# Performance work log

Hardware: AMD Instinct MI355X
Metric: run time of the kernel (lower is better)

The kernel has to match this reference:

```python
import jax, jax.numpy as jnp
import numpy as np

N_NODES = 30000
NEG_SLOPE = 0.2  # PyG GATConv default leaky_relu slope


def gat_conv(x, src, dst, W, a_src, a_dst, b, num_nodes, concat):
    """One PyG-style GATConv layer (add_self_loops already applied to src/dst).
    x: [N, F_in]; W: [F_in, H*C]; a_src, a_dst: [H, C]; b: [H*C] or [C].
    """
    H, C = a_src.shape
    h = (x @ W).reshape(num_nodes, H, C)                     # [N, H, C]
    alpha_src = jnp.einsum('nhc,hc->nh', h, a_src)           # [N, H]
    alpha_dst = jnp.einsum('nhc,hc->nh', h, a_dst)           # [N, H]
    e = jax.nn.leaky_relu(alpha_src[src] + alpha_dst[dst], NEG_SLOPE)  # [E, H]
    # scatter-softmax over incoming edges of each dst node
    e_max = jax.ops.segment_max(e, dst, num_segments=num_nodes)        # [N, H]
    e_exp = jnp.exp(e - e_max[dst])                                    # [E, H]
    denom = jax.ops.segment_sum(e_exp, dst, num_segments=num_nodes)    # [N, H]
    alpha = e_exp / denom[dst]                                         # [E, H]
    msg = h[src] * alpha[:, :, None]                                   # [E, H, C]
    out = jax.ops.segment_sum(msg, dst, num_segments=num_nodes)        # [N, H, C]
    out = out.reshape(num_nodes, H * C) if concat else out.mean(axis=1)
    return out + b


def _glorot(key, shape):
    fan = sum(shape[:2]) if len(shape) > 1 else shape[0] * 2
    return jax.random.normal(key, shape, dtype=jnp.float32) * np.sqrt(2.0 / fan)


def setup_inputs() -> dict:
    key = jax.random.key(0)
    ks = jax.random.split(key, 16)
    n, f_in, heads = N_NODES, 256, 4
    x = jax.random.normal(ks[0], (n, f_in), dtype=jnp.float32)
    edge_index = jax.random.randint(ks[1], (2, 480000), 0, n, dtype=jnp.int64)
    inp = {
        'x': x, 'edge_index': edge_index,
        'W1': _glorot(ks[2], (f_in, heads * 128)),
        'a1s': _glorot(ks[3], (heads, 128)), 'a1d': _glorot(ks[4], (heads, 128)),
        'b1': jnp.zeros((heads * 128,), jnp.float32),
        'W2': _glorot(ks[5], (heads * 128, heads * 128)),
        'a2s': _glorot(ks[6], (heads, 128)), 'a2d': _glorot(ks[7], (heads, 128)),
        'b2': jnp.zeros((heads * 128,), jnp.float32),
        'W3': _glorot(ks[8], (heads * 128, heads * 64)),
        'a3s': _glorot(ks[9], (heads, 64)), 'a3d': _glorot(ks[10], (heads, 64)),
        'b3': jnp.zeros((heads * 64,), jnp.float32),
        # conv4: 256 -> 64, 1 head, mean (concat=False)
        'W4': _glorot(ks[11], (heads * 64, 64)),
        'a4s': _glorot(ks[12], (1, 64)), 'a4d': _glorot(ks[13], (1, 64)),
        'b4': jnp.zeros((64,), jnp.float32),
    }
    return inp


def reference(x, edge_index, W1, a1s, a1d, b1, W2, a2s, a2d, b2,
              W3, a3s, a3d, b3, W4, a4s, a4d, b4):
    n = x.shape[0]
    # PyG GATConv default add_self_loops=True
    loops = jnp.arange(n, dtype=edge_index.dtype)
    src = jnp.concatenate([edge_index[0], loops])
    dst = jnp.concatenate([edge_index[1], loops])
    h = jax.nn.relu(gat_conv(x, src, dst, W1, a1s, a1d, b1, n, True))
    h = jax.nn.relu(gat_conv(h, src, dst, W2, a2s, a2d, b2, n, True))
    h = jax.nn.relu(gat_conv(h, src, dst, W3, a3s, a3d, b3, n, True))
    h = jax.nn.relu(gat_conv(h, src, dst, W4, a4s, a4d, b4, n, False))
    return h
```

## Files before the change

### kernel.cpp

```cpp
#include <hip/hip_runtime.h>
#include <hip/hip_fp16.h>
#include <math.h>


typedef __attribute__((ext_vector_type(8))) _Float16 f16x8;
typedef __attribute__((ext_vector_type(4))) float floatx4;
typedef __attribute__((ext_vector_type(8))) unsigned short usv8;
typedef __attribute__((ext_vector_type(4))) unsigned short usv4;

#define DEG_CAP 256

__device__ __forceinline__ float lrelu(float e) {
    return (e > 0.f) ? e : 0.2f * e;
}
__device__ __forceinline__ void gload16(const void* g, void* l) {
    __builtin_amdgcn_global_load_lds(
        (const __attribute__((address_space(1))) void*)g,
        (__attribute__((address_space(3))) void*)l, 16, 0, 0);
}

static __global__ void zero_int(int* __restrict__ p, int n) {
    int i = blockIdx.x * blockDim.x + threadIdx.x;
    if (i < n) p[i] = 0;
}

static __global__ void hist_kernel(const int* __restrict__ ei, int e0, int n_nodes,
                                   int* __restrict__ counts) {
    int e = blockIdx.x * blockDim.x + threadIdx.x;
    int et = e0 + n_nodes;
    if (e >= et) return;
    int d = (e < e0) ? ei[e0 + e] : (e - e0);
    atomicAdd(&counts[d], 1);
}

static __global__ void scan_kernel(const int* __restrict__ counts,
                                   int* __restrict__ row_ptr,
                                   int* __restrict__ cursor, int n) {
    __shared__ int sdata[1024];
    int tid = threadIdx.x;
    int per = (n + 1023) / 1024;
    int start = tid * per;
    int stop = min(start + per, n);
    if (start > n) start = n;
    int s = 0;
    for (int i = start; i < stop; i++) s += counts[i];
    sdata[tid] = s;
    __syncthreads();
    for (int off = 1; off < 1024; off <<= 1) {
        int t = (tid >= off) ? sdata[tid - off] : 0;
        __syncthreads();
        sdata[tid] += t;
        __syncthreads();
    }
    int run = sdata[tid] - s;
    for (int i = start; i < stop; i++) {
        row_ptr[i] = run;
        cursor[i] = run;
        run += counts[i];
    }
    if (stop == n) row_ptr[n] = run;
}

static __global__ void scatter_kernel(const int* __restrict__ ei, int e0, int n_nodes,
                                      int* __restrict__ cursor,
                                      int* __restrict__ src_sorted) {
    int e = blockIdx.x * blockDim.x + threadIdx.x;
    int et = e0 + n_nodes;
    if (e >= et) return;
    int s, d;
    if (e < e0) { s = ei[e]; d = ei[e0 + e]; } else { s = e - e0; d = s; }
    int pos = atomicAdd(&cursor[d], 1);
    src_sorted[pos] = s;
}

__device__ __forceinline__ void convW_one(const float* W, __half* BT,
                                          int idx, int K, int N) {
    int n = idx / K, k = idx % K;
    float v = (n < N) ? W[(size_t)k * N + n] : 0.f;
    BT[(size_t)n * K + k] = __float2half(v);
}

static __global__ void conv_all(const float* __restrict__ X, __half* __restrict__ A, int nx,
                                const float* __restrict__ W1, __half* __restrict__ BT1,
                                const float* __restrict__ W2, __half* __restrict__ BT2,
                                const float* __restrict__ W3, __half* __restrict__ BT3,
                                const float* __restrict__ W4, __half* __restrict__ BT4,
                                float* __restrict__ zero_as, int nzero) {
    int idx = blockIdx.x * 256 + threadIdx.x;
    if (idx < nx) { A[idx] = __float2half(X[idx]); return; }
    idx -= nx;
    if (idx < 131072) { convW_one(W1, BT1, idx, 256, 512); return; }
    idx -= 131072;
    if (idx < 262144) { convW_one(W2, BT2, idx, 512, 512); return; }
    idx -= 262144;
    if (idx < 131072) { convW_one(W3, BT3, idx, 512, 256); return; }
    idx -= 131072;
    if (idx < 32768)  { convW_one(W4, BT4, idx, 256, 64); return; }
    idx -= 32768;
    if (idx < nzero) zero_as[idx] = 0.f;
}

#define BM 128
#define BN 128
#define BKK 64

__launch_bounds__(256, 4)
static __global__ void gemm_mfma(const __half* __restrict__ A,
                                 const __half* __restrict__ B,
                                 __half* __restrict__ C, int M, int K, int N,
                                 int xcols, int mblocks,
                                 const float* __restrict__ asv,
                                 const float* __restrict__ adv,
                                 float* __restrict__ as_out,
                                 float* __restrict__ ad_out,
                                 int Hh, int Cc) {
    __shared__ __align__(16) __half lds[2 * BM * BKK];
    const int tid  = threadIdx.x;
    const int lane = tid & 63;
    const int wave = tid >> 6;

    const int id = blockIdx.x;
    const int band = id / (8 * xcols);
    const int rem = id - band * 8 * xcols;
    const int band_rows = min(8, mblocks - band * 8);
    const int ry = rem % band_rows;
    const int rx = rem / band_rows;
    const int r0 = (band * 8 + ry) * BM;
    const int c0 = rx * BN;

    const int wm = (wave >> 1) * 64;
    const int wn = (wave & 1) * 64;
    const int q   = lane >> 4;
    const int m16 = lane & 15;

    floatx4 acc[4][4];
#pragma unroll
    for (int i = 0; i < 4; i++)
#pragma unroll
        for (int j = 0; j < 4; j++) acc[i][j] = {0.f, 0.f, 0.f, 0.f};

    char* ldsb = (char*)lds;

#pragma unroll 1
    for (int k0 = 0; k0 < K; k0 += BKK) {
        __syncthreads();
#pragma unroll
        for (int c = 0; c < 4; c++) {
            int slot = c * 256 + tid;
            int row = slot >> 3;
            int gc  = (slot & 7) ^ (row & 7);
            gload16(A + (size_t)(r0 + row) * K + k0 + gc * 8,
                    ldsb + slot * 16);
            gload16(B + (size_t)(c0 + row) * K + k0 + gc * 8,
                    ldsb + 16384 + slot * 16);
        }
        __syncthreads();
#pragma unroll
        for (int ks = 0; ks < 2; ks++) {
            f16x8 af[4], bf[4];
#pragma unroll
            for (int i = 0; i < 4; i++) {
                int row = wm + i * 16 + m16;
                int ch  = (q + ks * 4) ^ (row & 7);
                af[i] = *(const f16x8*)(ldsb + (row * 8 + ch) * 16);
            }
#pragma unroll
            for (int j = 0; j < 4; j++) {
                int row = wn + j * 16 + m16;
                int ch  = (q + ks * 4) ^ (row & 7);
                bf[j] = *(const f16x8*)(ldsb + 16384 + (row * 8 + ch) * 16);
            }
#pragma unroll
            for (int i = 0; i < 4; i++)
#pragma unroll
                for (int j = 0; j < 4; j++)
                    acc[i][j] = __builtin_amdgcn_mfma_f32_16x16x32_f16(
                        af[i], bf[j], acc[i][j], 0, 0, 0);
        }
    }
#pragma unroll
    for (int i = 0; i < 4; i++)
#pragma unroll
        for (int j = 0; j < 4; j++)
#pragma unroll
            for (int r = 0; r < 4; r++) {
                int row = r0 + wm + i * 16 + q * 4 + r;
                int col = c0 + wn + j * 16 + m16;
                if (row < M && col < N)
                    C[(size_t)row * N + col] = __float2half(acc[i][j][r]);
            }
    if (c0 + wn < N) {
        int head = (c0 + wn) / Cc;
#pragma unroll
        for (int i = 0; i < 4; i++)
#pragma unroll
            for (int r = 0; r < 4; r++) {
                float ps = 0.f, pd = 0.f;
#pragma unroll
                for (int j = 0; j < 4; j++) {
                    int c = c0 + wn + j * 16 + m16;
                    float v = acc[i][j][r];
                    ps = fmaf(v, asv[c], ps);
                    pd = fmaf(v, adv[c], pd);
                }
#pragma unroll
                for (int off = 1; off < 16; off <<= 1) {
                    ps += __shfl_xor(ps, off);
                    pd += __shfl_xor(pd, off);
                }
                if (m16 == 0) {
                    int row = r0 + wm + i * 16 + q * 4 + r;
                    if (row < M) {
                        atomicAdd(&as_out[(size_t)row * Hh + head], ps);
                        atomicAdd(&ad_out[(size_t)row * Hh + head], pd);
                    }
                }
            }
    }
}

template <int R>
__device__ __forceinline__ void accum_row(const __half* hptr, size_t off, float w,
                                          float* acc) {
    const __half* p = hptr + off;
    if constexpr (R == 8) {
        float4 raw = *(const float4*)p;
        const __half* hv = (const __half*)&raw;
#pragma unroll
        for (int r = 0; r < 8; r++) acc[r] = fmaf(__half2float(hv[r]), w, acc[r]);
    } else if constexpr (R == 4) {
        float2 raw = *(const float2*)p;
        const __half* hv = (const __half*)&raw;
#pragma unroll
        for (int r = 0; r < 4; r++) acc[r] = fmaf(__half2float(hv[r]), w, acc[r]);
    } else {
        acc[0] = fmaf(__half2float(*p), w, acc[0]);
    }
}

template <int H, int C, bool F16OUT>
__launch_bounds__(256)
static __global__ void agg_kernel(const __half* __restrict__ h,
                                  const float* __restrict__ as_arr,
                                  const float* __restrict__ ad_arr,
                                  const int* __restrict__ row_ptr,
                                  const int* __restrict__ src_sorted,
                                  const float* __restrict__ bias,
                                  float* __restrict__ outf,
                                  __half* __restrict__ outh,
                                  float* __restrict__ znext_as,
                                  float* __restrict__ znext_ad, int n_nodes) {
    constexpr int R = H * C / 64;
    constexpr int G = 64 / H;
    constexpr int K = H * C;
    __shared__ float lds_e[4][DEG_CAP * H];
    int wave = threadIdx.x >> 6;
    int lane = threadIdx.x & 63;
    int n = blockIdx.x * 4 + wave;
    if (n >= n_nodes) return;
    int beg = row_ptr[n], end = row_ptr[n + 1];
    float* we = lds_e[wave];

    float ad_h[H], m_h[H], l_h[H];
#pragma unroll
    for (int hh = 0; hh < H; hh++) {
        ad_h[hh] = ad_arr[(size_t)n * H + hh];
        m_h[hh] = -INFINITY;
        l_h[hh] = 0.f;
    }
    for (int base = beg; base < end; base += 64) {
        int j = base + lane;
        bool ok = j < end;
        float e_h[H];
        if (ok) {
            int s = src_sorted[j];
            if constexpr (H == 4) {
                float4 a = ((const float4*)as_arr)[s];
                e_h[0] = lrelu(a.x + ad_h[0]);
                e_h[1] = lrelu(a.y + ad_h[1]);
                e_h[2] = lrelu(a.z + ad_h[2]);
                e_h[3] = lrelu(a.w + ad_h[3]);
            } else {
                e_h[0] = lrelu(as_arr[s] + ad_h[0]);
            }
            int idx = j - beg;
            if (idx < DEG_CAP) {
                if constexpr (H == 4) {
                    *(float4*)&we[idx * 4] = make_float4(e_h[0], e_h[1], e_h[2], e_h[3]);
                } else {
                    we[idx] = e_h[0];
                }
            }
        } else {
#pragma unroll
            for (int hh = 0; hh < H; hh++) e_h[hh] = -INFINITY;
        }
#pragma unroll
        for (int hh = 0; hh < H; hh++) {
            float cm = e_h[hh];
#pragma unroll
            for (int off = 1; off < 64; off <<= 1) cm = fmaxf(cm, __shfl_xor(cm, off));
            float newm = fmaxf(m_h[hh], cm);
            float p = ok ? __expf(e_h[hh] - newm) : 0.f;
#pragma unroll
            for (int off = 1; off < 64; off <<= 1) p += __shfl_xor(p, off);
            l_h[hh] = l_h[hh] * __expf(m_h[hh] - newm) + p;
            m_h[hh] = newm;
        }
    }
    int myh = lane / G;
    float mm, adm, inv;
    if constexpr (H == 4) {
        mm  = m_h[0];  mm  = (myh == 1) ? m_h[1] : mm;  mm  = (myh == 2) ? m_h[2] : mm;  mm  = (myh == 3) ? m_h[3] : mm;
        float ll = l_h[0]; ll = (myh == 1) ? l_h[1] : ll; ll = (myh == 2) ? l_h[2] : ll; ll = (myh == 3) ? l_h[3] : ll;
        adm = ad_h[0]; adm = (myh == 1) ? ad_h[1] : adm; adm = (myh == 2) ? ad_h[2] : adm; adm = (myh == 3) ? ad_h[3] : adm;
        inv = 1.f / ll;
    } else {
        mm = m_h[0]; adm = ad_h[0]; inv = 1.f / l_h[0];
    }

    float acc[R];
#pragma unroll
    for (int r = 0; r < R; r++) acc[r] = 0.f;

    int j = beg;
    for (; j + 3 < end; j += 4) {
        int i0 = j - beg;
        int s0 = src_sorted[j];
        int s1 = src_sorted[j + 1];
        int s2 = src_sorted[j + 2];
        int s3 = src_sorted[j + 3];
        float e0, e1, e2, e3;
        if (i0 + 3 < DEG_CAP) {
            e0 = we[(i0 + 0) * H + myh];
            e1 = we[(i0 + 1) * H + myh];
            e2 = we[(i0 + 2) * H + myh];
            e3 = we[(i0 + 3) * H + myh];
        } else {
            e0 = lrelu(as_arr[(size_t)s0 * H + myh] + adm);
            e1 = lrelu(as_arr[(size_t)s1 * H + myh] + adm);
            e2 = lrelu(as_arr[(size_t)s2 * H + myh] + adm);
            e3 = lrelu(as_arr[(size_t)s3 * H + myh] + adm);
        }
        float w0 = __expf(e0 - mm) * inv;
        float w1 = __expf(e1 - mm) * inv;
        float w2 = __expf(e2 - mm) * inv;
        float w3 = __expf(e3 - mm) * inv;
        accum_row<R>(h, (size_t)s0 * K + lane * R, w0, acc);
        accum_row<R>(h, (size_t)s1 * K + lane * R, w1, acc);
        accum_row<R>(h, (size_t)s2 * K + lane * R, w2, acc);
        accum_row<R>(h, (size_t)s3 * K + lane * R, w3, acc);
    }
    for (; j < end; j++) {
        int i0 = j - beg;
        int s0 = src_sorted[j];
        float e0 = (i0 < DEG_CAP) ? we[i0 * H + myh]
                                  : lrelu(as_arr[(size_t)s0 * H + myh] + adm);
        float w0 = __expf(e0 - mm) * inv;
        accum_row<R>(h, (size_t)s0 * K + lane * R, w0, acc);
    }

    if (znext_as != nullptr && lane == 0) {
        if constexpr (H == 4) {
            *(float4*)&znext_as[(size_t)n * 4] = make_float4(0.f, 0.f, 0.f, 0.f);
            *(float4*)&znext_ad[(size_t)n * 4] = make_float4(0.f, 0.f, 0.f, 0.f);
        } else {
            znext_as[n] = 0.f;
            znext_ad[n] = 0.f;
        }
    }
    float vout[R];
#pragma unroll
    for (int r = 0; r < R; r++)
        vout[r] = fmaxf(acc[r] + bias[lane * R + r], 0.f);

    if constexpr (F16OUT) {
        unsigned short hv[R];
#pragma unroll
        for (int r = 0; r < R; r++)
            hv[r] = __half_as_ushort(__float2half(vout[r]));
        size_t base = (size_t)n * K + lane * R;
        if constexpr (R == 8) {
            usv8 v = {hv[0], hv[1], hv[2], hv[3], hv[4], hv[5], hv[6], hv[7]};
            *(usv8*)((unsigned short*)outh + base) = v;
        } else if constexpr (R == 4) {
            usv4 v = {hv[0], hv[1], hv[2], hv[3]};
            *(usv4*)((unsigned short*)outh + base) = v;
        } else {
#pragma unroll
            for (int r = 0; r < R; r++) ((unsigned short*)outh)[base + r] = hv[r];
        }
    } else {
#pragma unroll
        for (int r = 0; r < R; r++)
            outf[(size_t)n * K + lane * R + r] = vout[r];
    }
}


static inline size_t align_up(size_t x) { return (x + 255) & ~(size_t)255; }

extern "C" void kernel_launch(void* const* d_in, const int* in_sizes, int n_in,
                              void* d_out, int out_size, void* d_ws, size_t ws_size,
                              hipStream_t stream) {
    const float* x   = (const float*)d_in[0];
    const int*   ei  = (const int*)d_in[1];
    const float* W1  = (const float*)d_in[2];
    const float* a1s = (const float*)d_in[3];
    const float* a1d = (const float*)d_in[4];
    const float* b1  = (const float*)d_in[5];
    const float* W2  = (const float*)d_in[6];
    const float* a2s = (const float*)d_in[7];
    const float* a2d = (const float*)d_in[8];
    const float* b2  = (const float*)d_in[9];
    const float* W3  = (const float*)d_in[10];
    const float* a3s = (const float*)d_in[11];
    const float* a3d = (const float*)d_in[12];
    const float* b3  = (const float*)d_in[13];
    const float* W4  = (const float*)d_in[14];
    const float* a4s = (const float*)d_in[15];
    const float* a4d = (const float*)d_in[16];
    const float* b4  = (const float*)d_in[17];

    const int n  = in_sizes[0] / 256;
    const int e0 = in_sizes[1] / 2;
    const int et = e0 + n;
    const int Mpad = ((n + 127) / 128) * 128;

    char* w = (char*)d_ws;
    __half* bufA = (__half*)w;                   w += align_up((size_t)Mpad * 512 * 2);
    __half* bufB = (__half*)w;                   w += align_up((size_t)Mpad * 512 * 2);
    __half* hbuf = (__half*)w;                   w += align_up((size_t)Mpad * 512 * 2);
    __half* WT1 = (__half*)w;                    w += align_up((size_t)512 * 256 * 2);
    __half* WT2 = (__half*)w;                    w += align_up((size_t)512 * 512 * 2);
    __half* WT3 = (__half*)w;                    w += align_up((size_t)256 * 512 * 2);
    __half* WT4 = (__half*)w;                    w += align_up((size_t)128 * 256 * 2);
    float* asA = (float*)w;                      w += align_up((size_t)n * 4 * 4);
    float* adA = (float*)w;                      w += align_up((size_t)n * 4 * 4);
    float* asB = (float*)w;                      w += align_up((size_t)n * 4 * 4);
    float* adB = (float*)w;                      w += align_up((size_t)n * 4 * 4);
    int* row_ptr = (int*)w;                      w += align_up((size_t)(n + 1) * 4);
    int* counts  = (int*)w;                      w += align_up((size_t)n * 4);
    int* cursor  = (int*)w;                      w += align_up((size_t)n * 4);
    int* src_sorted = (int*)w;                   w += align_up((size_t)et * 4);
    (void)ws_size;

    dim3 blk(256);
    int nodeblocks = (n + 3) / 4;

    zero_int<<<(n + 255) / 256, 256, 0, stream>>>(counts, n);
    hist_kernel<<<(et + 255) / 256, 256, 0, stream>>>(ei, e0, n, counts);
    scan_kernel<<<1, 1024, 0, stream>>>(counts, row_ptr, cursor, n);
    scatter_kernel<<<(et + 255) / 256, 256, 0, stream>>>(ei, e0, n, cursor, src_sorted);

    const int nx = n * 256;
    conv_all<<<(nx + 557056 + n * 8 + 255) / 256, blk, 0, stream>>>(
        x, bufA, nx, W1, WT1, W2, WT2, W3, WT3, W4, WT4, asA, n * 8);

    const int mblocks = Mpad / 128;

    gemm_mfma<<<dim3(4 * mblocks), blk, 0, stream>>>(bufA, WT1, hbuf, n, 256, 512, 4, mblocks,
                                                     a1s, a1d, asA, adA, 4, 128);
    agg_kernel<4, 128, true><<<nodeblocks, blk, 0, stream>>>(hbuf, asA, adA, row_ptr, src_sorted, b1, nullptr, bufB, asB, adB, n);

    gemm_mfma<<<dim3(4 * mblocks), blk, 0, stream>>>(bufB, WT2, hbuf, n, 512, 512, 4, mblocks,
                                                     a2s, a2d, asB, adB, 4, 128);
    agg_kernel<4, 128, true><<<nodeblocks, blk, 0, stream>>>(hbuf, asB, adB, row_ptr, src_sorted, b2, nullptr, bufA, asA, adA, n);

    gemm_mfma<<<dim3(2 * mblocks), blk, 0, stream>>>(bufA, WT3, hbuf, n, 512, 256, 2, mblocks,
                                                     a3s, a3d, asA, adA, 4, 64);
    agg_kernel<4, 64, true><<<nodeblocks, blk, 0, stream>>>(hbuf, asA, adA, row_ptr, src_sorted, b3, nullptr, bufB, asB, adB, n);

    gemm_mfma<<<dim3(1 * mblocks), blk, 0, stream>>>(bufB, WT4, hbuf, n, 256, 64, 1, mblocks,
                                                     a4s, a4d, asB, adB, 1, 64);
    agg_kernel<1, 64, false><<<nodeblocks, blk, 0, stream>>>(hbuf, asB, adB, row_ptr, src_sorted, b4, (float*)d_out, nullptr, nullptr, nullptr, n);
}
```

Measured before the change: 559.5 us.

## Split GAT aggregation into softmax-weight pass and column-sliced gather pass

Replaces the fused per-node aggregation kernel with two kernels. The first computes normalized attention weights per edge and stores them as fp16. The second gathers neighbour features in 64-column slices, one column per lane, with each wave handling 8 nodes. The intent is better cache locality, since each slice touches a narrower footprint of h. In exchange it adds an extra pass and a weight buffer write and read. The gather now issues scalar 2-byte loads instead of 16-byte vector loads.

```diff
diff --git a/kernel.cpp b/kernel.cpp
--- a/kernel.cpp
+++ b/kernel.cpp
@@ -17,6 +17,11 @@
     __builtin_amdgcn_global_load_lds(
         (const __attribute__((address_space(1))) void*)g,
         (__attribute__((address_space(3))) void*)l, 16, 0, 0);
+}
+__device__ __forceinline__ float ushort2floath(unsigned short u) {
+    union { unsigned short u; __half h; } cv;
+    cv.u = u;
+    return __half2float(cv.h);
 }
 
 static __global__ void zero_int(int* __restrict__ p, int n) {
@@ -219,40 +224,15 @@
     }
 }
 
-template <int R>
-__device__ __forceinline__ void accum_row(const __half* hptr, size_t off, float w,
-                                          float* acc) {
-    const __half* p = hptr + off;
-    if constexpr (R == 8) {
-        float4 raw = *(const float4*)p;
-        const __half* hv = (const __half*)&raw;
-#pragma unroll
-        for (int r = 0; r < 8; r++) acc[r] = fmaf(__half2float(hv[r]), w, acc[r]);
-    } else if constexpr (R == 4) {
-        float2 raw = *(const float2*)p;
-        const __half* hv = (const __half*)&raw;
-#pragma unroll
-        for (int r = 0; r < 4; r++) acc[r] = fmaf(__half2float(hv[r]), w, acc[r]);
-    } else {
-        acc[0] = fmaf(__half2float(*p), w, acc[0]);
-    }
-}
-
-template <int H, int C, bool F16OUT>
+template <int H>
 __launch_bounds__(256)
-static __global__ void agg_kernel(const __half* __restrict__ h,
-                                  const float* __restrict__ as_arr,
-                                  const float* __restrict__ ad_arr,
-                                  const int* __restrict__ row_ptr,
-                                  const int* __restrict__ src_sorted,
-                                  const float* __restrict__ bias,
-                                  float* __restrict__ outf,
-                                  __half* __restrict__ outh,
-                                  float* __restrict__ znext_as,
-                                  float* __restrict__ znext_ad, int n_nodes) {
-    constexpr int R = H * C / 64;
-    constexpr int G = 64 / H;
-    constexpr int K = H * C;
+static __global__ void stats_kernel(const float* __restrict__ as_arr,
+                                    const float* __restrict__ ad_arr,
+                                    const int* __restrict__ row_ptr,
+                                    const int* __restrict__ src_sorted,
+                                    __half* __restrict__ w_arr,
+                                    float* __restrict__ znext_as,
+                                    float* __restrict__ znext_ad, int n_nodes) {
     __shared__ float lds_e[4][DEG_CAP * H];
     int wave = threadIdx.x >> 6;
     int lane = threadIdx.x & 63;
@@ -308,56 +288,48 @@
             m_h[hh] = newm;
         }
     }
-    int myh = lane / G;
-    float mm, adm, inv;
-    if constexpr (H == 4) {
-        mm  = m_h[0];  mm  = (myh == 1) ? m_h[1] : mm;  mm  = (myh == 2) ? m_h[2] : mm;  mm  = (myh == 3) ? m_h[3] : mm;
-        float ll = l_h[0]; ll = (myh == 1) ? l_h[1] : ll; ll = (myh == 2) ? l_h[2] : ll; ll = (myh == 3) ? l_h[3] : ll;
-        adm = ad_h[0]; adm = (myh == 1) ? ad_h[1] : adm; adm = (myh == 2) ? ad_h[2] : adm; adm = (myh == 3) ? ad_h[3] : adm;
-        inv = 1.f / ll;
-    } else {
-        mm = m_h[0]; adm = ad_h[0]; inv = 1.f / l_h[0];
-    }
-
-    float acc[R];
-#pragma unroll
-    for (int r = 0; r < R; r++) acc[r] = 0.f;
-
-    int j = beg;
-    for (; j + 3 < end; j += 4) {
-        int i0 = j - beg;
-        int s0 = src_sorted[j];
-        int s1 = src_sorted[j + 1];
-        int s2 = src_sorted[j + 2];
-        int s3 = src_sorted[j + 3];
-        float e0, e1, e2, e3;
-        if (i0 + 3 < DEG_CAP) {
-            e0 = we[(i0 + 0) * H + myh];
-            e1 = we[(i0 + 1) * H + myh];
-            e2 = we[(i0 + 2) * H + myh];
-            e3 = we[(i0 + 3) * H + myh];
-        } else {
-            e0 = lrelu(as_arr[(size_t)s0 * H + myh] + adm);
-            e1 = lrelu(as_arr[(size_t)s1 * H + myh] + adm);
-            e2 = lrelu(as_arr[(size_t)s2 * H + myh] + adm);
-            e3 = lrelu(as_arr[(size_t)s3 * H + myh] + adm);
-        }
-        float w0 = __expf(e0 - mm) * inv;
-        float w1 = __expf(e1 - mm) * inv;
-        float w2 = __expf(e2 - mm) * inv;
-        float w3 = __expf(e3 - mm) * inv;
-        accum_row<R>(h, (size_t)s0 * K + lane * R, w0, acc);
-        accum_row<R>(h, (size_t)s1 * K + lane * R, w1, acc);
-        accum_row<R>(h, (size_t)s2 * K + lane * R, w2, acc);
-        accum_row<R>(h, (size_t)s3 * K + lane * R, w3, acc);
-    }
-    for (; j < end; j++) {
-        int i0 = j - beg;
-        int s0 = src_sorted[j];
-        float e0 = (i0 < DEG_CAP) ? we[i0 * H + myh]
-                                  : lrelu(as_arr[(size_t)s0 * H + myh] + adm);
-        float w0 = __expf(e0 - mm) * inv;
-        accum_row<R>(h, (size_t)s0 * K + lane * R, w0, acc);
+    float inv_h[H];
+#pragma unroll
+    for (int hh = 0; hh < H; hh++) inv_h[hh] = 1.f / l_h[hh];
+
+    for (int base = beg; base < end; base += 64) {
+        int j = base + lane;
+        if (j < end) {
+            int idx = j - beg;
+            float e_h[H];
+            if (idx < DEG_CAP) {
+                if constexpr (H == 4) {
+                    float4 t = *(float4*)&we[idx * 4];
+                    e_h[0] = t.x; e_h[1] = t.y; e_h[2] = t.z; e_h[3] = t.w;
+                } else {
+                    e_h[0] = we[idx];
+                }
+            } else {
+                int s = src_sorted[j];
+                if constexpr (H == 4) {
+                    float4 a = ((const float4*)as_arr)[s];
+                    e_h[0] = lrelu(a.x + ad_h[0]);
+                    e_h[1] = lrelu(a.y + ad_h[1]);
+                    e_h[2] = lrelu(a.z + ad_h[2]);
+                    e_h[3] = lrelu(a.w + ad_h[3]);
+                } else {
+                    e_h[0] = lrelu(as_arr[s] + ad_h[0]);
+                }
+            }
+            if constexpr (H == 4) {
+                usv4 v;
+#pragma unroll
+                for (int hh = 0; hh < 4; hh++)
+                    v[hh] = __half_as_ushort(
+                        __float2half(__expf(e_h[hh] - m_h[hh]) * inv_h[hh]));
+                __builtin_nontemporal_store(
+                    v, (usv4*)((unsigned short*)w_arr + (size_t)j * 4));
+            } else {
+                unsigned short u = __half_as_ushort(
+                    __float2half(__expf(e_h[0] - m_h[0]) * inv_h[0]));
+                __builtin_nontemporal_store(u, (unsigned short*)w_arr + j);
+            }
+        }
     }
 
     if (znext_as != nullptr && lane == 0) {
@@ -369,31 +341,68 @@
             znext_ad[n] = 0.f;
         }
     }
-    float vout[R];
-#pragma unroll
-    for (int r = 0; r < R; r++)
-        vout[r] = fmaxf(acc[r] + bias[lane * R + r], 0.f);
-
-    if constexpr (F16OUT) {
-        unsigned short hv[R];
-#pragma unroll
-        for (int r = 0; r < R; r++)
-            hv[r] = __half_as_ushort(__float2half(vout[r]));
-        size_t base = (size_t)n * K + lane * R;
-        if constexpr (R == 8) {
-            usv8 v = {hv[0], hv[1], hv[2], hv[3], hv[4], hv[5], hv[6], hv[7]};
-            *(usv8*)((unsigned short*)outh + base) = v;
-        } else if constexpr (R == 4) {
-            usv4 v = {hv[0], hv[1], hv[2], hv[3]};
-            *(usv4*)((unsigned short*)outh + base) = v;
+}
+
+template <int H, int C, bool F16OUT>
+__launch_bounds__(256)
+static __global__ void gather_slice(const __half* __restrict__ h,
+                                    const __half* __restrict__ w_arr,
+                                    const int* __restrict__ row_ptr,
+                                    const int* __restrict__ src_sorted,
+                                    const float* __restrict__ bias,
+                                    float* __restrict__ outf,
+                                    __half* __restrict__ outh, int n_nodes) {
+    constexpr int K = H * C;
+    constexpr int NSLICE = K / 64;
+    constexpr int NPW = 8;
+    const int wave = threadIdx.x >> 6;
+    const int lane = threadIdx.x & 63;
+    const int slice = blockIdx.x % NSLICE;
+    const int group = blockIdx.x / NSLICE;
+    const int col = slice * 64 + lane;
+    const int head = col / C;
+    const float bcol = bias[col];
+    const unsigned short* wp = (const unsigned short*)w_arr;
+
+    int n0 = (group * 4 + wave) * NPW;
+    for (int ni = 0; ni < NPW; ni++) {
+        int n = n0 + ni;
+        if (n >= n_nodes) return;
+        int beg = row_ptr[n], end = row_ptr[n + 1];
+        float acc = 0.f;
+        int j = beg;
+        for (; j + 3 < end; j += 4) {
+            int s0 = __builtin_nontemporal_load(src_sorted + j);
+            int s1 = __builtin_nontemporal_load(src_sorted + j + 1);
+            int s2 = __builtin_nontemporal_load(src_sorted + j + 2);
+            int s3 = __builtin_nontemporal_load(src_sorted + j + 3);
+            float w0 = ushort2floath(
+                __builtin_nontemporal_load(wp + (size_t)(j + 0) * H + head));
+            float w1 = ushort2floath(
+                __builtin_nontemporal_load(wp + (size_t)(j + 1) * H + head));
+            float w2 = ushort2floath(
+                __builtin_nontemporal_load(wp + (size_t)(j + 2) * H + head));
+            float w3 = ushort2floath(
+                __builtin_nontemporal_load(wp + (size_t)(j + 3) * H + head));
+            acc = fmaf(w0, __half2float(h[(size_t)s0 * K + col]), acc);
+            acc = fmaf(w1, __half2float(h[(size_t)s1 * K + col]), acc);
+            acc = fmaf(w2, __half2float(h[(size_t)s2 * K + col]), acc);
+            acc = fmaf(w3, __half2float(h[(size_t)s3 * K + col]), acc);
+        }
+        for (; j < end; j++) {
+            int s0 = __builtin_nontemporal_load(src_sorted + j);
+            float w0 = ushort2floath(
+                __builtin_nontemporal_load(wp + (size_t)j * H + head));
+            acc = fmaf(w0, __half2float(h[(size_t)s0 * K + col]), acc);
+        }
+        float v = fmaxf(acc + bcol, 0.f);
+        if constexpr (F16OUT) {
+            __builtin_nontemporal_store(
+                __half_as_ushort(__float2half(v)),
+                (unsigned short*)outh + (size_t)n * K + col);
         } else {
-#pragma unroll
-            for (int r = 0; r < R; r++) ((unsigned short*)outh)[base + r] = hv[r];
-        }
-    } else {
-#pragma unroll
-        for (int r = 0; r < R; r++)
-            outf[(size_t)n * K + lane * R + r] = vout[r];
+            __builtin_nontemporal_store(v, outf + (size_t)n * K + col);
+        }
     }
 }
 
@@ -443,10 +452,12 @@
     int* counts  = (int*)w;                      w += align_up((size_t)n * 4);
     int* cursor  = (int*)w;                      w += align_up((size_t)n * 4);
     int* src_sorted = (int*)w;                   w += align_up((size_t)et * 4);
+    __half* wbuf = (__half*)w;                   w += align_up((size_t)et * 4 * 2);
     (void)ws_size;
 
     dim3 blk(256);
     int nodeblocks = (n + 3) / 4;
+    int ggrp = (n + 31) / 32;
 
     zero_int<<<(n + 255) / 256, 256, 0, stream>>>(counts, n);
     hist_kernel<<<(et + 255) / 256, 256, 0, stream>>>(ei, e0, n, counts);
@@ -461,17 +472,25 @@
 
     gemm_mfma<<<dim3(4 * mblocks), blk, 0, stream>>>(bufA, WT1, hbuf, n, 256, 512, 4, mblocks,
                                                      a1s, a1d, asA, adA, 4, 128);
-    agg_kernel<4, 128, true><<<nodeblocks, blk, 0, stream>>>(hbuf, asA, adA, row_ptr, src_sorted, b1, nullptr, bufB, asB, adB, n);
+    stats_kernel<4><<<nodeblocks, blk, 0, stream>>>(asA, adA, row_ptr, src_sorted, wbuf, asB, adB, n);
+    gather_slice<4, 128, true><<<dim3(8 * ggrp), blk, 0, stream>>>(
+        hbuf, wbuf, row_ptr, src_sorted, b1, nullptr, bufB, n);
 
     gemm_mfma<<<dim3(4 * mblocks), blk, 0, stream>>>(bufB, WT2, hbuf, n, 512, 512, 4, mblocks,
                                                      a2s, a2d, asB, adB, 4, 128);
-    agg_kernel<4, 128, true><<<nodeblocks, blk, 0, stream>>>(hbuf, asB, adB, row_ptr, src_sorted, b2, nullptr, bufA, asA, adA, n);
+    stats_kernel<4><<<nodeblocks, blk, 0, stream>>>(asB, adB, row_ptr, src_sorted, wbuf, asA, adA, n);
+    gather_slice<4, 128, true><<<dim3(8 * ggrp), blk, 0, stream>>>(
+        hbuf, wbuf, row_ptr, src_sorted, b2, nullptr, bufA, n);
 
     gemm_mfma<<<dim3(2 * mblocks), blk, 0, stream>>>(bufA, WT3, hbuf, n, 512, 256, 2, mblocks,
                                                      a3s, a3d, asA, adA, 4, 64);
-    agg_kernel<4, 64, true><<<nodeblocks, blk, 0, stream>>>(hbuf, asA, adA, row_ptr, src_sorted, b3, nullptr, bufB, asB, adB, n);
+    stats_kernel<4><<<nodeblocks, blk, 0, stream>>>(asA, adA, row_ptr, src_sorted, wbuf, asB, adB, n);
+    gather_slice<4, 64, true><<<dim3(4 * ggrp), blk, 0, stream>>>(
+        hbuf, wbuf, row_ptr, src_sorted, b3, nullptr, bufB, n);
 
     gemm_mfma<<<dim3(1 * mblocks), blk, 0, stream>>>(bufB, WT4, hbuf, n, 256, 64, 1, mblocks,
                                                      a4s, a4d, asB, adB, 1, 64);
-    agg_kernel<1, 64, false><<<nodeblocks, blk, 0, stream>>>(hbuf, asB, adB, row_ptr, src_sorted, b4, (float*)d_out, nullptr, nullptr, nullptr, n);
-}
+    stats_kernel<1><<<nodeblocks, blk, 0, stream>>>(asB, adB, row_ptr, src_sorted, wbuf, nullptr, nullptr, n);
+    gather_slice<1, 64, false><<<dim3(1 * ggrp), blk, 0, stream>>>(
+        hbuf, wbuf, row_ptr, src_sorted, b4, (float*)d_out, nullptr, n);
+}
```

Result: slower. 989.3 us (+76.8%).
